# Kernel optimization log

Measured on AMD Instinct MI355X. Metric: run time of the kernel, lower is better.

Reference implementation:

```python
import jax, jax.numpy as jnp
import numpy as np

B, T, C, H = 4, 2048, 1024, 16
D = C // H


def setup_inputs() -> dict:
    key = jax.random.key(0)
    ks = jax.random.split(key, 5)
    s = C ** -0.5  # keep linear outputs O(1) like standard init
    x = jax.random.normal(ks[0], (B, T, C), dtype=jnp.float32)
    Wq = jax.random.normal(ks[1], (C, C), dtype=jnp.float32) * s
    Wk = jax.random.normal(ks[2], (C, C), dtype=jnp.float32) * s
    Wv = jax.random.normal(ks[3], (C, C), dtype=jnp.float32) * s
    Wproj = jax.random.normal(ks[4], (C, C), dtype=jnp.float32) * s
    alpha_raw = jnp.zeros((1, H, 1, 1), dtype=jnp.float32)
    beta_raw = jnp.zeros((1, H, 1, 1), dtype=jnp.float32)
    state = jnp.zeros((B, H, D, D), dtype=jnp.float32)
    return dict(x=x, Wq=Wq, Wk=Wk, Wv=Wv, Wproj=Wproj,
                alpha_raw=alpha_raw, beta_raw=beta_raw, state=state)


def reference(x, Wq, Wk, Wv, Wproj, alpha_raw, beta_raw, state):
    Bx, Tx, Cx = x.shape
    Hn = alpha_raw.shape[1]
    Dh = Cx // Hn
    # projections (torch Linear: x @ W^T), split heads -> (B, H, T, D)
    def proj(W):
        return (x @ W.T).reshape(Bx, Tx, Hn, Dh).transpose(0, 2, 1, 3)
    q, k, v = proj(Wq), proj(Wk), proj(Wv)
    # F.normalize(k, dim=-1) with eps=1e-12
    k = k / jnp.maximum(jnp.linalg.norm(k, axis=-1, keepdims=True), 1e-12)
    alpha = jax.nn.sigmoid(alpha_raw) * 0.5  # (1, H, 1, 1)
    beta = jax.nn.sigmoid(beta_raw) * 0.5

    def step(st, qkv):
        qt, kt, vt = qkv  # each (B, H, D)
        # y_t = q_t @ state^T
        y = jnp.einsum('bhe,bhde->bhd', qt, st)
        # Mk = state @ k_t
        Mk = jnp.einsum('bhde,bhe->bhd', st, kt)
        st = st - alpha * jnp.einsum('bhd,bhe->bhde', Mk, kt) \
                + beta * jnp.einsum('bhd,bhe->bhde', vt, kt)
        return st, y

    # scan over time: (T, B, H, D)
    qT = q.transpose(2, 0, 1, 3)
    kT = k.transpose(2, 0, 1, 3)
    vT = v.transpose(2, 0, 1, 3)
    state_f, ys = jax.lax.scan(step, state, (qT, kT, vT))
    y = ys.transpose(1, 0, 2, 3).reshape(Bx, Tx, Cx)  # (B, T, C)
    out = y @ Wproj.T
    return out, state_f
```

## Files before the change

kernel.cpp:

```cpp
#include <hip/hip_runtime.h>
#include <hip/hip_bf16.h>
#include <cstdint>

#define B_ 4
#define T_ 2048
#define C_ 1024
#define H_ 16
#define D_ 64
#define NC_ 32
#define L_ 64

typedef __attribute__((ext_vector_type(8))) short bf16x8;
typedef __attribute__((ext_vector_type(4))) float f32x4;

static __device__ __forceinline__ unsigned short f2bf(float f) {
  unsigned u = __float_as_uint(f);
  u += 0x7fff + ((u >> 16) & 1);
  return (unsigned short)(u >> 16);
}
static __device__ __forceinline__ float bf2f(unsigned short b) {
  return __uint_as_float(((unsigned)b) << 16);
}
static __device__ __forceinline__ int swz128(int row, int byte) {
  return row * 128 + (byte ^ ((row & 7) << 4));
}

#define LDS_BARRIER() asm volatile("s_waitcnt lgkmcnt(0)\ns_barrier" ::: "memory")

__global__ __launch_bounds__(256) void cvt_all(const float* __restrict__ x,
                                               const float* __restrict__ wq,
                                               const float* __restrict__ wk,
                                               const float* __restrict__ wv,
                                               const float* __restrict__ wp,
                                               unsigned short* __restrict__ xbf,
                                               unsigned short* __restrict__ W3,
                                               unsigned short* __restrict__ Wp) {
  const int bidx = blockIdx.x;
  const float* src;
  unsigned short* dst;
  long base;
  if (bidx < 8192) {
    src = x; dst = xbf; base = (long)bidx * 1024;
  } else {
    const int g = (bidx - 8192) >> 10;
    src = (g == 0) ? wq : (g == 1) ? wk : (g == 2) ? wv : wp;
    dst = (g < 3) ? (W3 + (long)g * 1048576) : Wp;
    base = (long)((bidx - 8192) & 1023) * 1024;
  }
  long i = base + threadIdx.x * 4;
  float4 v = *reinterpret_cast<const float4*>(src + i);
  ushort4 o;
  o.x = f2bf(v.x); o.y = f2bf(v.y); o.z = f2bf(v.z); o.w = f2bf(v.w);
  *reinterpret_cast<ushort4*>(dst + i) = o;
}

#define STAGE256(GP, GR0, KT, LOFF) do {                                          \
    const unsigned short* _s = (GP) + ((GR0) + wid * 8 + lr8) * 1024L             \
                               + (long)(KT) * 64 + skb * 8;                       \
    char* _d = (char*)lds + (LOFF) + wid * 1024;                                  \
    __builtin_amdgcn_global_load_lds((const __attribute__((address_space(1))) void*)_s,      \
        (__attribute__((address_space(3))) void*)_d, 16, 0, 0);                   \
    __builtin_amdgcn_global_load_lds((const __attribute__((address_space(1))) void*)(_s + 64 * 1024L), \
        (__attribute__((address_space(3))) void*)(_d + 8192), 16, 0, 0);          \
  } while (0)

#define PHASE256(AO, BO, MH, NH, STG) do {                                        \
    asm volatile("s_waitcnt vmcnt(6)" ::: "memory");                              \
    bf16x8 av[4][2], bv[2][2];                                                    \
    {                                                                             \
      const char* ab = (const char*)lds + (AO) + (MH) * 16384 + arow;             \
      const char* bb = (const char*)lds + (BO) + (NH) * 16384 + brow;             \
      _Pragma("unroll")                                                           \
      for (int j = 0; j < 4; ++j) {                                               \
        av[j][0] = *(const bf16x8*)(ab + j * 4096 + cb0);                         \
        av[j][1] = *(const bf16x8*)(ab + j * 4096 + cb1);                         \
      }                                                                           \
      _Pragma("unroll")                                                           \
      for (int j2 = 0; j2 < 2; ++j2) {                                            \
        bv[j2][0] = *(const bf16x8*)(bb + j2 * 8192 + cb0);                       \
        bv[j2][1] = *(const bf16x8*)(bb + j2 * 8192 + cb1);                       \
      }                                                                           \
    }                                                                             \
    STG;                                                                          \
    __builtin_amdgcn_s_barrier();                                                 \
    asm volatile("s_waitcnt lgkmcnt(0)" ::: "memory");                            \
    __builtin_amdgcn_sched_barrier(0);                                            \
    __builtin_amdgcn_s_setprio(1);                                                \
    _Pragma("unroll")                                                             \
    for (int j = 0; j < 4; ++j)                                                   \
      _Pragma("unroll")                                                           \
      for (int j2 = 0; j2 < 2; ++j2)                                              \
        acc[(MH) * 4 + j][(NH) * 2 + j2] = __builtin_amdgcn_mfma_f32_16x16x32_bf16( \
            av[j][0], bv[j2][0], acc[(MH) * 4 + j][(NH) * 2 + j2], 0, 0, 0);      \
    _Pragma("unroll")                                                             \
    for (int j = 0; j < 4; ++j)                                                   \
      _Pragma("unroll")                                                           \
      for (int j2 = 0; j2 < 2; ++j2)                                              \
        acc[(MH) * 4 + j][(NH) * 2 + j2] = __builtin_amdgcn_mfma_f32_16x16x32_bf16( \
            av[j][1], bv[j2][1], acc[(MH) * 4 + j][(NH) * 2 + j2], 0, 0, 0);      \
    __builtin_amdgcn_s_setprio(0);                                                \
    __builtin_amdgcn_s_barrier();                                                 \
  } while (0)

__global__ __launch_bounds__(512, 2) void gemm256_bt(
    const unsigned short* __restrict__ A,
    const unsigned short* __restrict__ Bw,
    unsigned short* __restrict__ C, int N) {
  __shared__ __align__(16) char lds[131072];
  enum { EA = 0, EB = 32768, OA = 65536, OB = 98304, HF = 16384 };
  const int tid = threadIdx.x;
  const int wid = tid >> 6, lane = tid & 63;
  const int wm = wid >> 2, wn = wid & 3;
  const int f = lane & 15, g = lane >> 4;
  const int lr8 = lane >> 3, lc = lane & 7;
  const int skb = lc ^ lr8;
  const int bid = blockIdx.y * gridDim.x + blockIdx.x;
  const int cpx = (gridDim.x * gridDim.y) >> 3;
  const int sw = (bid & 7) * cpx + (bid >> 3);
  const long bM = (long)(sw / gridDim.x) * 256;
  const long bN = (long)(sw % gridDim.x) * 256;
  const int cb0 = ((0 + g) ^ (f & 7)) * 16;
  const int cb1 = ((4 + g) ^ (f & 7)) * 16;
  const int arow = (wm * 16 + f) * 128;
  const int brow = (wn * 16 + f) * 128;

  f32x4 acc[8][4] = {};

  STAGE256(A, bM, 0, EA);
  STAGE256(Bw, bN, 0, EB);
  STAGE256(A, bM + 128, 0, EA + HF);
  STAGE256(Bw, bN + 128, 0, EB + HF);
  STAGE256(Bw, bN, 1, OB);
  STAGE256(A, bM, 1, OA);
  asm volatile("s_waitcnt vmcnt(8)" ::: "memory");
  __builtin_amdgcn_s_barrier();

  for (int i = 0; i < 8; ++i) {
    const int todd = 2 * i + 1;
    int te = 2 * i + 2; if (te > 14) te = 14;
    int to = 2 * i + 3; if (to > 15) to = 15;
    PHASE256(EA, EB, 0, 0, STAGE256(A, bM + 128, todd, OA + HF));
    PHASE256(EA, EB, 1, 0, STAGE256(Bw, bN + 128, todd, OB + HF));
    PHASE256(EA, EB, 0, 1, STAGE256(Bw, bN, te, EB));
    PHASE256(EA, EB, 1, 1, STAGE256(A, bM, te, EA));
    PHASE256(OA, OB, 0, 0, STAGE256(A, bM + 128, te, EA + HF));
    PHASE256(OA, OB, 1, 0, STAGE256(Bw, bN + 128, te, EB + HF));
    PHASE256(OA, OB, 0, 1, STAGE256(Bw, bN, to, OB));
    PHASE256(OA, OB, 1, 1, STAGE256(A, bM, to, OA));
  }

#pragma unroll
  for (int mf = 0; mf < 8; ++mf) {
    long row = bM + (mf >> 2) * 128 + (mf & 3) * 32 + wm * 16 + g * 4;
#pragma unroll
    for (int nf = 0; nf < 4; ++nf) {
      long col = bN + (nf >> 1) * 128 + (nf & 1) * 64 + wn * 16 + f;
#pragma unroll
      for (int r = 0; r < 4; ++r)
        C[(row + r) * (long)N + col] = f2bf(acc[mf][nf][r]);
    }
  }
}

template<int OUT_BF16>
__global__ __launch_bounds__(256) void gemm_bt(const unsigned short* __restrict__ A,
                                               const unsigned short* __restrict__ Bw,
                                               void* __restrict__ Cp,
                                               int M, int N, int K) {
  __shared__ __align__(16) unsigned short sA[128 * 32];
  __shared__ __align__(16) unsigned short sB[128 * 32];
  const int tid = threadIdx.x;
  const int wid = tid >> 6, lane = tid & 63;
  const int wm = wid >> 1, wn = wid & 1;
  const int bid = blockIdx.y * gridDim.x + blockIdx.x;
  const int cpx = (gridDim.x * gridDim.y) >> 3;
  const int sw = (bid & 7) * cpx + (bid >> 3);
  const long blockM = (long)(sw / gridDim.x) * 128;
  const long blockN = (long)(sw % gridDim.x) * 128;

  f32x4 acc[4][4] = {};

  const int ar = lane >> 2;
  const int ac = (lane & 3) * 8;
  const unsigned short* Abase = A + (blockM + wid * 32 + ar) * (long)K + ac;
  const unsigned short* Bbase = Bw + (blockN + wid * 32 + ar) * (long)K + ac;
  char* sAb = (char*)sA + wid * 2048;
  char* sBb = (char*)sB + wid * 2048;

  for (int k0 = 0; k0 < K; k0 += 32) {
    __syncthreads();
    __builtin_amdgcn_global_load_lds((const __attribute__((address_space(1))) void*)(Abase + k0),
                                     (__attribute__((address_space(3))) void*)(sAb), 16, 0, 0);
    __builtin_amdgcn_global_load_lds((const __attribute__((address_space(1))) void*)(Abase + 16 * (long)K + k0),
                                     (__attribute__((address_space(3))) void*)(sAb + 1024), 16, 0, 0);
    __builtin_amdgcn_global_load_lds((const __attribute__((address_space(1))) void*)(Bbase + k0),
                                     (__attribute__((address_space(3))) void*)(sBb), 16, 0, 0);
    __builtin_amdgcn_global_load_lds((const __attribute__((address_space(1))) void*)(Bbase + 16 * (long)K + k0),
                                     (__attribute__((address_space(3))) void*)(sBb + 1024), 16, 0, 0);
    __syncthreads();

    const int koff = (lane >> 4) * 8;
    const int rA = wm * 64 + (lane & 15);
    const int rB = wn * 64 + (lane & 15);
    bf16x8 af[4], bfr[4];
#pragma unroll
    for (int m = 0; m < 4; ++m)
      af[m] = *reinterpret_cast<const bf16x8*>(&sA[(rA + m * 16) * 32 + koff]);
#pragma unroll
    for (int n = 0; n < 4; ++n)
      bfr[n] = *reinterpret_cast<const bf16x8*>(&sB[(rB + n * 16) * 32 + koff]);
#pragma unroll
    for (int m = 0; m < 4; ++m)
#pragma unroll
      for (int n = 0; n < 4; ++n)
        acc[m][n] = __builtin_amdgcn_mfma_f32_16x16x32_bf16(af[m], bfr[n], acc[m][n], 0, 0, 0);
  }

  const int cr = (lane >> 4) * 4;
  const int cc = lane & 15;
#pragma unroll
  for (int m = 0; m < 4; ++m) {
    long R = blockM + wm * 64 + m * 16 + cr;
#pragma unroll
    for (int n = 0; n < 4; ++n) {
      long Cc = blockN + wn * 64 + n * 16 + cc;
#pragma unroll
      for (int r = 0; r < 4; ++r) {
        if (OUT_BF16)
          ((unsigned short*)Cp)[(R + r) * (long)N + Cc] = f2bf(acc[m][n][r]);
        else
          ((float*)Cp)[(R + r) * (long)N + Cc] = acc[m][n][r];
      }
    }
  }
}

__global__ __launch_bounds__(256) void chunk_prep(
    unsigned short* __restrict__ qkv,
    const float* __restrict__ a_raw, const float* __restrict__ b_raw,
    unsigned short* __restrict__ Ubuf, unsigned short* __restrict__ Wbuf,
    unsigned short* __restrict__ SLbuf) {
  __shared__ __align__(16) unsigned short sK[64 * 64];
  __shared__ __align__(16) unsigned short sQ[64 * 64];
  __shared__ __align__(16) unsigned short sV[64 * 64];
  __shared__ float sA[64 * 64];

  const int blk = blockIdx.x;
  const int bh = blk >> 5, c = blk & 31;
  const int b = bh >> 4, h = bh & 15;
  const int tid = threadIdx.x;
  const int wid = tid >> 6, lane = tid & 63;

  const float alpha = 0.5f / (1.f + __expf(-a_raw[h]));
  const float beta  = 0.5f / (1.f + __expf(-b_raw[h]));

  {
    const int row = tid >> 2, cg = tid & 3;
    unsigned short* gp = qkv + (long)(b * 2048 + c * 64 + row) * 3072 + h * 64 + cg * 16;
    bf16x8 q0 = *(const bf16x8*)(gp);
    bf16x8 q1 = *(const bf16x8*)(gp + 8);
    bf16x8 k0 = *(const bf16x8*)(gp + 1024);
    bf16x8 k1 = *(const bf16x8*)(gp + 1024 + 8);
    bf16x8 v0 = *(const bf16x8*)(gp + 2048);
    bf16x8 v1 = *(const bf16x8*)(gp + 2048 + 8);
    float kf[16];
    float ss = 0.f;
#pragma unroll
    for (int i = 0; i < 8; ++i) { kf[i] = bf2f((unsigned short)k0[i]); ss += kf[i] * kf[i]; }
#pragma unroll
    for (int i = 0; i < 8; ++i) { kf[8 + i] = bf2f((unsigned short)k1[i]); ss += kf[8 + i] * kf[8 + i]; }
    ss += __shfl_xor(ss, 1);
    ss += __shfl_xor(ss, 2);
    const float inv = 1.f / fmaxf(sqrtf(ss), 1e-12f);
    bf16x8 n0, n1;
#pragma unroll
    for (int i = 0; i < 8; ++i) { n0[i] = (short)f2bf(kf[i] * inv); n1[i] = (short)f2bf(kf[8 + i] * inv); }
    *(bf16x8*)((char*)sK + swz128(row, cg * 32)) = n0;
    *(bf16x8*)((char*)sK + swz128(row, cg * 32 + 16)) = n1;
    *(bf16x8*)((char*)sQ + swz128(row, cg * 32)) = q0;
    *(bf16x8*)((char*)sQ + swz128(row, cg * 32 + 16)) = q1;
    *(bf16x8*)((char*)sV + row * 128 + cg * 32) = v0;
    *(bf16x8*)((char*)sV + row * 128 + cg * 32 + 16) = v1;
  }
  __syncthreads();

  {
    const int erow = tid >> 2, tq = tid & 3;
    unsigned short kt[16];
#pragma unroll
    for (int i = 0; i < 16; ++i)
      kt[i] = *(const unsigned short*)((const char*)sK + swz128(tq * 16 + i, 2 * erow));
    unsigned short* vp = qkv + (long)(b * 2048 + c * 64 + erow) * 3072 + 2048 + h * 64 + tq * 16;
    *(bf16x8*)vp = *(const bf16x8*)kt;
    *(bf16x8*)(vp + 8) = *(const bf16x8*)(kt + 8);
  }

  const int rfrag = lane & 15, koff = (lane >> 4) * 8, crow = (lane >> 4) * 4;
  const int w2 = wid & 1;
  if (wid < 2) {
#pragma unroll
    for (int mt = 0; mt < 2; ++mt) {
      const int m = w2 * 2 + mt;
      const int ra = 16 * m + rfrag;
      f32x4 acc[4] = {};
#pragma unroll
      for (int ks = 0; ks < 2; ++ks) {
        bf16x8 af = *(const bf16x8*)((const char*)sK + swz128(ra, ks * 64 + koff * 2));
#pragma unroll
        for (int n = 0; n < 4; ++n) {
          bf16x8 bf = *(const bf16x8*)((const char*)sK + swz128(16 * n + rfrag, ks * 64 + koff * 2));
          acc[n] = __builtin_amdgcn_mfma_f32_16x16x32_bf16(af, bf, acc[n], 0, 0, 0);
        }
      }
#pragma unroll
      for (int n = 0; n < 4; ++n)
#pragma unroll
        for (int r = 0; r < 4; ++r)
          sA[(16 * m + crow + r) * 64 + 16 * n + rfrag] = acc[n][r];
    }
  } else {
#pragma unroll
    for (int mt = 0; mt < 2; ++mt) {
      const int m = w2 * 2 + mt;
      const int ra = 16 * m + rfrag;
      f32x4 acc[4] = {};
#pragma unroll
      for (int ks = 0; ks < 2; ++ks) {
        bf16x8 af = *(const bf16x8*)((const char*)sQ + swz128(ra, ks * 64 + koff * 2));
#pragma unroll
        for (int n = 0; n < 4; ++n) {
          bf16x8 bf = *(const bf16x8*)((const char*)sK + swz128(16 * n + rfrag, ks * 64 + koff * 2));
          acc[n] = __builtin_amdgcn_mfma_f32_16x16x32_bf16(af, bf, acc[n], 0, 0, 0);
        }
      }
#pragma unroll
      for (int n = 0; n < 4; ++n)
#pragma unroll
        for (int r = 0; r < 4; ++r) {
          int t = 16 * m + crow + r, j = 16 * n + rfrag;
          SLbuf[(long)blk * 4096 + t * 64 + j] = (j < t) ? f2bf(acc[n][r]) : (unsigned short)0;
        }
    }
  }
  __syncthreads();

  if (wid < 2) {
    const int d = lane;
    float x[64];
#pragma unroll
    for (int t = 0; t < 64; ++t) {
      float rhs;
      if (wid == 0) rhs = beta * bf2f(sV[t * 64 + d]);
      else          rhs = alpha * bf2f(*(const unsigned short*)((const char*)sK + swz128(t, 2 * d)));
      float s = 0.f;
#pragma unroll
      for (int j = 0; j < t; ++j) s = fmaf(sA[t * 64 + j], x[j], s);
      x[t] = rhs - alpha * s;
    }
    unsigned short* ob = (wid == 0 ? Ubuf : Wbuf) + (long)blk * 4096 + d;
#pragma unroll
    for (int t = 0; t < 64; ++t) ob[t * 64] = f2bf(x[t]);
  }
}

__global__ __launch_bounds__(256) void chunk_scan(
    const unsigned short* __restrict__ qkv,
    const unsigned short* __restrict__ Ubuf, const unsigned short* __restrict__ Wbuf,
    const unsigned short* __restrict__ SLbuf,
    const float* __restrict__ state_in, unsigned short* __restrict__ ybuf,
    float* __restrict__ state_out) {
  __shared__ __align__(16) char lds[73728];

  const int bid0 = blockIdx.x;
  const int blk = (bid0 & 7) * 32 + (bid0 >> 3);
  const int bh = blk >> 2, dq = blk & 3;
  const int b = bh >> 4, h = bh & 15;
  const int tid = threadIdx.x, wid = tid >> 6, lane = tid & 63;
  const int rfrag = lane & 15, koff = (lane >> 4) * 8, crow = (lane >> 4) * 4;
  const int row = tid >> 2, cg = tid & 3;

  char* gt = lds + 69632;
  char* ssb = lds + 71680;

  const unsigned short* gpb = qkv + (long)(b * 2048 + row) * 3072 + h * 64 + cg * 16;
  const long tbb = ((long)(bh * 32) * 64 + row) * 64 + cg * 16;
  const long ubb = ((long)(bh * 32) * 64 + (tid >> 1)) * 64 + dq * 16 + (tid & 1) * 8;

  bf16x8 qv0, qv1, kt0, kt1, wv0, wv1, sl0, sl1, uv;
#define LOADREGS(CN) do {                                                       \
    const unsigned short* gp = gpb + (long)(CN) * 64 * 3072;                    \
    const long tb = tbb + (long)(CN) * 4096;                                    \
    qv0 = *(const bf16x8*)gp;            qv1 = *(const bf16x8*)(gp + 8);        \
    kt0 = *(const bf16x8*)(gp + 2048);   kt1 = *(const bf16x8*)(gp + 2048 + 8); \
    wv0 = *(const bf16x8*)(Wbuf + tb);   wv1 = *(const bf16x8*)(Wbuf + tb + 8); \
    sl0 = *(const bf16x8*)(SLbuf + tb);  sl1 = *(const bf16x8*)(SLbuf + tb + 8);\
    if (tid < 128) uv = *(const bf16x8*)(Ubuf + ubb + (long)(CN) * 4096);       \
  } while (0)

#define WRITE_TILES(BUF) do {                                                   \
    char* bp = lds + (BUF) * 34816;                                             \
    *(bf16x8*)(bp + swz128(row, cg * 32)) = qv0;                                \
    *(bf16x8*)(bp + swz128(row, cg * 32 + 16)) = qv1;                           \
    *(bf16x8*)(bp + 8192 + swz128(row, cg * 32)) = wv0;                         \
    *(bf16x8*)(bp + 8192 + swz128(row, cg * 32 + 16)) = wv1;                    \
    *(bf16x8*)(bp + 16384 + swz128(row, cg * 32)) = sl0;                        \
    *(bf16x8*)(bp + 16384 + swz128(row, cg * 32 + 16)) = sl1;                   \
    *(bf16x8*)(bp + 24576 + swz128(row, cg * 32)) = kt0;                        \
    *(bf16x8*)(bp + 24576 + swz128(row, cg * 32 + 16)) = kt1;                   \
    if (tid < 128) *(bf16x8*)(bp + 32768 + ((tid >> 1) * 16 + (tid & 1) * 8) * 2) = uv; \
  } while (0)

  f32x4 sacc;
#pragma unroll
  for (int r = 0; r < 4; ++r)
    sacc[r] = state_in[(long)bh * 4096 + (dq * 16 + crow + r) * 64 + 16 * wid + rfrag];
#pragma unroll
  for (int r = 0; r < 4; ++r)
    *(unsigned short*)(ssb + swz128(crow + r, 2 * (16 * wid + rfrag))) = f2bf(sacc[r]);

  LOADREGS(0);
  WRITE_TILES(0);
  LOADREGS(1);
  LDS_BARRIER();

  for (int c = 0; c < NC_; ++c) {
    const int cur = c & 1;
    const char* bp = lds + cur * 34816;
    const int ta = 16 * wid + rfrag;

    f32x4 p = {};
    f32x4 yac = {};
#pragma unroll
    for (int ks = 0; ks < 2; ++ks) {
      bf16x8 afw = *(const bf16x8*)(bp + 8192 + swz128(ta, ks * 64 + koff * 2));
      bf16x8 afq = *(const bf16x8*)(bp + swz128(ta, ks * 64 + koff * 2));
      bf16x8 bS = *(const bf16x8*)(ssb + swz128(rfrag, ks * 64 + koff * 2));
      p = __builtin_amdgcn_mfma_f32_16x16x32_bf16(afw, bS, p, 0, 0, 0);
      yac = __builtin_amdgcn_mfma_f32_16x16x32_bf16(afq, bS, yac, 0, 0, 0);
    }
#pragma unroll
    for (int r = 0; r < 4; ++r) {
      int t = 16 * wid + crow + r;
      float gg = bf2f(*(const unsigned short*)(bp + 32768 + (t * 16 + rfrag) * 2)) - p[r];
      *(unsigned short*)(gt + swz128(rfrag, 2 * t)) = f2bf(gg);
    }
    LDS_BARRIER();

#pragma unroll
    for (int ks = 0; ks < 2; ++ks) {
      bf16x8 aSL = *(const bf16x8*)(bp + 16384 + swz128(ta, ks * 64 + koff * 2));
      bf16x8 bGT = *(const bf16x8*)(gt + swz128(rfrag, ks * 64 + koff * 2));
      yac = __builtin_amdgcn_mfma_f32_16x16x32_bf16(aSL, bGT, yac, 0, 0, 0);
    }
#pragma unroll
    for (int ks = 0; ks < 2; ++ks) {
      bf16x8 aGT = *(const bf16x8*)(gt + swz128(rfrag, ks * 64 + koff * 2));
      bf16x8 bKT = *(const bf16x8*)(bp + 24576 + swz128(16 * wid + rfrag, ks * 64 + koff * 2));
      sacc = __builtin_amdgcn_mfma_f32_16x16x32_bf16(aGT, bKT, sacc, 0, 0, 0);
    }
#pragma unroll
    for (int r = 0; r < 4; ++r) {
      int t = 16 * wid + crow + r;
      ybuf[(long)(b * 2048 + c * 64 + t) * 1024 + h * 64 + dq * 16 + rfrag] = f2bf(yac[r]);
    }
#pragma unroll
    for (int r = 0; r < 4; ++r)
      *(unsigned short*)(ssb + swz128(crow + r, 2 * (16 * wid + rfrag))) = f2bf(sacc[r]);
    if (c + 1 < NC_) {
      WRITE_TILES(cur ^ 1);
      int cn = c + 2; if (cn > NC_ - 1) cn = NC_ - 1;
      LOADREGS(cn);
    }
    LDS_BARRIER();
  }

#pragma unroll
  for (int r = 0; r < 4; ++r)
    state_out[(long)bh * 4096 + (dq * 16 + crow + r) * 64 + 16 * wid + rfrag] = sacc[r];
#undef LOADREGS
#undef WRITE_TILES
}

extern "C" void kernel_launch(void* const* d_in, const int* in_sizes, int n_in,
                              void* d_out, int out_size, void* d_ws, size_t ws_size,
                              hipStream_t stream) {
  (void)in_sizes; (void)n_in; (void)out_size; (void)ws_size;
  const float* x     = (const float*)d_in[0];
  const float* Wq    = (const float*)d_in[1];
  const float* Wk    = (const float*)d_in[2];
  const float* Wv    = (const float*)d_in[3];
  const float* Wproj = (const float*)d_in[4];
  const float* a_raw = (const float*)d_in[5];
  const float* b_raw = (const float*)d_in[6];
  const float* state = (const float*)d_in[7];

  char* ws = (char*)d_ws;
  unsigned short* xbf = (unsigned short*)ws;
  unsigned short* W3  = (unsigned short*)(ws + (16l << 20));
  unsigned short* Wp  = (unsigned short*)(ws + (22l << 20));
  unsigned short* qkv = (unsigned short*)(ws + (24l << 20));
  unsigned short* Ub  = (unsigned short*)(ws + (72l << 20));
  unsigned short* Wb  = (unsigned short*)(ws + (88l << 20));
  unsigned short* SLb = (unsigned short*)(ws + (104l << 20));
  float* out = (float*)d_out;
  float* state_out = out + (long)B_ * T_ * C_;

  cvt_all<<<dim3(12288), dim3(256), 0, stream>>>(x, Wq, Wk, Wv, Wproj, xbf, W3, Wp);

  gemm256_bt<<<dim3(3072 / 256, 8192 / 256), dim3(512), 0, stream>>>(xbf, W3, qkv, 3072);

  chunk_prep<<<dim3(2048), dim3(256), 0, stream>>>(qkv, a_raw, b_raw, Ub, Wb, SLb);
  chunk_scan<<<dim3(256), dim3(256), 0, stream>>>(qkv, Ub, Wb, SLb, state, xbf, state_out);

  gemm_bt<0><<<dim3(1024 / 128, 8192 / 128), dim3(256), 0, stream>>>(xbf, Wp, (void*)out, 8192, 1024, 1024);
}
```

Baseline: 180.8 us.

## Merge four d-quarter scan blocks per head into one 1024-thread block sharing tiles

The chunk scan previously launched 256 blocks of 256 threads, with four blocks per (batch, head) each redundantly loading the same Q, K, W and SL chunk tiles. It now launches 64 blocks of 1024 threads, one per (batch, head). The four d-quarters run as wave groups within the block and share one copy of the staged tiles, and each thread loads a single tile slice. This removes the fourfold redundant global loads and LDS staging. In exchange only 64 CUs are used, the block-wide barriers now span 16 waves, and LDS use per block grows.

```diff
diff --git a/kernel.cpp b/kernel.cpp
--- a/kernel.cpp
+++ b/kernel.cpp
@@ -363,60 +363,59 @@
   }
 }
 
-__global__ __launch_bounds__(256) void chunk_scan(
+__global__ __launch_bounds__(1024) void chunk_scan(
     const unsigned short* __restrict__ qkv,
     const unsigned short* __restrict__ Ubuf, const unsigned short* __restrict__ Wbuf,
     const unsigned short* __restrict__ SLbuf,
     const float* __restrict__ state_in, unsigned short* __restrict__ ybuf,
     float* __restrict__ state_out) {
-  __shared__ __align__(16) char lds[73728];
+  __shared__ __align__(16) char lds[98304];
 
   const int bid0 = blockIdx.x;
-  const int blk = (bid0 & 7) * 32 + (bid0 >> 3);
-  const int bh = blk >> 2, dq = blk & 3;
+  const int bh = (bid0 & 7) * 8 + (bid0 >> 3);
   const int b = bh >> 4, h = bh & 15;
-  const int tid = threadIdx.x, wid = tid >> 6, lane = tid & 63;
+  const int tid = threadIdx.x;
+  const int wid = tid >> 6, lane = tid & 63;
+  const int dq = wid >> 2, w4 = wid & 3;
   const int rfrag = lane & 15, koff = (lane >> 4) * 8, crow = (lane >> 4) * 4;
-  const int row = tid >> 2, cg = tid & 3;
-
-  char* gt = lds + 69632;
-  char* ssb = lds + 71680;
-
-  const unsigned short* gpb = qkv + (long)(b * 2048 + row) * 3072 + h * 64 + cg * 16;
-  const long tbb = ((long)(bh * 32) * 64 + row) * 64 + cg * 16;
-  const long ubb = ((long)(bh * 32) * 64 + (tid >> 1)) * 64 + dq * 16 + (tid & 1) * 8;
-
-  bf16x8 qv0, qv1, kt0, kt1, wv0, wv1, sl0, sl1, uv;
+
+  const int stile = tid >> 8, srow = (tid >> 2) & 63, scg = tid & 3;
+  const int tg = tid & 255, ur = tg >> 1, uh = tg & 1;
+
+  char* gt  = lds + 81920 + dq * 2048;
+  char* ssb = lds + 90112 + dq * 2048;
+
+  const unsigned short* gsrc0;
+  long gstride;
+  if (stile == 0)      { gsrc0 = qkv + (long)(b * 2048 + srow) * 3072 + h * 64 + scg * 16; gstride = 64 * 3072; }
+  else if (stile == 1) { gsrc0 = Wbuf + ((long)(bh * 32) * 64 + srow) * 64 + scg * 16; gstride = 4096; }
+  else if (stile == 2) { gsrc0 = SLbuf + ((long)(bh * 32) * 64 + srow) * 64 + scg * 16; gstride = 4096; }
+  else                 { gsrc0 = qkv + (long)(b * 2048 + srow) * 3072 + 2048 + h * 64 + scg * 16; gstride = 64 * 3072; }
+  const unsigned short* usrc0 = Ubuf + ((long)(bh * 32) * 64 + ur) * 64 + dq * 16 + uh * 8;
+
+  bf16x8 rv0 = {}, rv1 = {}, uv = {};
 #define LOADREGS(CN) do {                                                       \
-    const unsigned short* gp = gpb + (long)(CN) * 64 * 3072;                    \
-    const long tb = tbb + (long)(CN) * 4096;                                    \
-    qv0 = *(const bf16x8*)gp;            qv1 = *(const bf16x8*)(gp + 8);        \
-    kt0 = *(const bf16x8*)(gp + 2048);   kt1 = *(const bf16x8*)(gp + 2048 + 8); \
-    wv0 = *(const bf16x8*)(Wbuf + tb);   wv1 = *(const bf16x8*)(Wbuf + tb + 8); \
-    sl0 = *(const bf16x8*)(SLbuf + tb);  sl1 = *(const bf16x8*)(SLbuf + tb + 8);\
-    if (tid < 128) uv = *(const bf16x8*)(Ubuf + ubb + (long)(CN) * 4096);       \
+    const unsigned short* gp = gsrc0 + (long)(CN) * gstride;                    \
+    rv0 = *(const bf16x8*)gp;                                                   \
+    rv1 = *(const bf16x8*)(gp + 8);                                             \
+    if (tg < 128) uv = *(const bf16x8*)(usrc0 + (long)(CN) * 4096);             \
   } while (0)
 
 #define WRITE_TILES(BUF) do {                                                   \
-    char* bp = lds + (BUF) * 34816;                                             \
-    *(bf16x8*)(bp + swz128(row, cg * 32)) = qv0;                                \
-    *(bf16x8*)(bp + swz128(row, cg * 32 + 16)) = qv1;                           \
-    *(bf16x8*)(bp + 8192 + swz128(row, cg * 32)) = wv0;                         \
-    *(bf16x8*)(bp + 8192 + swz128(row, cg * 32 + 16)) = wv1;                    \
-    *(bf16x8*)(bp + 16384 + swz128(row, cg * 32)) = sl0;                        \
-    *(bf16x8*)(bp + 16384 + swz128(row, cg * 32 + 16)) = sl1;                   \
-    *(bf16x8*)(bp + 24576 + swz128(row, cg * 32)) = kt0;                        \
-    *(bf16x8*)(bp + 24576 + swz128(row, cg * 32 + 16)) = kt1;                   \
-    if (tid < 128) *(bf16x8*)(bp + 32768 + ((tid >> 1) * 16 + (tid & 1) * 8) * 2) = uv; \
+    char* bp_ = lds + (BUF) * 32768 + stile * 8192;                             \
+    *(bf16x8*)(bp_ + swz128(srow, scg * 32)) = rv0;                             \
+    *(bf16x8*)(bp_ + swz128(srow, scg * 32 + 16)) = rv1;                        \
+    if (tg < 128)                                                               \
+      *(bf16x8*)(lds + 65536 + dq * 4096 + (BUF) * 2048 + (ur * 16 + uh * 8) * 2) = uv; \
   } while (0)
 
   f32x4 sacc;
 #pragma unroll
   for (int r = 0; r < 4; ++r)
-    sacc[r] = state_in[(long)bh * 4096 + (dq * 16 + crow + r) * 64 + 16 * wid + rfrag];
+    sacc[r] = state_in[(long)bh * 4096 + (dq * 16 + crow + r) * 64 + 16 * w4 + rfrag];
 #pragma unroll
   for (int r = 0; r < 4; ++r)
-    *(unsigned short*)(ssb + swz128(crow + r, 2 * (16 * wid + rfrag))) = f2bf(sacc[r]);
+    *(unsigned short*)(ssb + swz128(crow + r, 2 * (16 * w4 + rfrag))) = f2bf(sacc[r]);
 
   LOADREGS(0);
   WRITE_TILES(0);
@@ -425,8 +424,9 @@
 
   for (int c = 0; c < NC_; ++c) {
     const int cur = c & 1;
-    const char* bp = lds + cur * 34816;
-    const int ta = 16 * wid + rfrag;
+    const char* bp = lds + cur * 32768;
+    const char* up = lds + 65536 + dq * 4096 + cur * 2048;
+    const int ta = 16 * w4 + rfrag;
 
     f32x4 p = {};
     f32x4 yac = {};
@@ -440,8 +440,8 @@
     }
 #pragma unroll
     for (int r = 0; r < 4; ++r) {
-      int t = 16 * wid + crow + r;
-      float gg = bf2f(*(const unsigned short*)(bp + 32768 + (t * 16 + rfrag) * 2)) - p[r];
+      int t = 16 * w4 + crow + r;
+      float gg = bf2f(*(const unsigned short*)(up + (t * 16 + rfrag) * 2)) - p[r];
       *(unsigned short*)(gt + swz128(rfrag, 2 * t)) = f2bf(gg);
     }
     LDS_BARRIER();
@@ -455,17 +455,17 @@
 #pragma unroll
     for (int ks = 0; ks < 2; ++ks) {
       bf16x8 aGT = *(const bf16x8*)(gt + swz128(rfrag, ks * 64 + koff * 2));
-      bf16x8 bKT = *(const bf16x8*)(bp + 24576 + swz128(16 * wid + rfrag, ks * 64 + koff * 2));
+      bf16x8 bKT = *(const bf16x8*)(bp + 24576 + swz128(16 * w4 + rfrag, ks * 64 + koff * 2));
       sacc = __builtin_amdgcn_mfma_f32_16x16x32_bf16(aGT, bKT, sacc, 0, 0, 0);
     }
 #pragma unroll
     for (int r = 0; r < 4; ++r) {
-      int t = 16 * wid + crow + r;
+      int t = 16 * w4 + crow + r;
       ybuf[(long)(b * 2048 + c * 64 + t) * 1024 + h * 64 + dq * 16 + rfrag] = f2bf(yac[r]);
     }
 #pragma unroll
     for (int r = 0; r < 4; ++r)
-      *(unsigned short*)(ssb + swz128(crow + r, 2 * (16 * wid + rfrag))) = f2bf(sacc[r]);
+      *(unsigned short*)(ssb + swz128(crow + r, 2 * (16 * w4 + rfrag))) = f2bf(sacc[r]);
     if (c + 1 < NC_) {
       WRITE_TILES(cur ^ 1);
       int cn = c + 2; if (cn > NC_ - 1) cn = NC_ - 1;
@@ -476,7 +476,7 @@
 
 #pragma unroll
   for (int r = 0; r < 4; ++r)
-    state_out[(long)bh * 4096 + (dq * 16 + crow + r) * 64 + 16 * wid + rfrag] = sacc[r];
+    state_out[(long)bh * 4096 + (dq * 16 + crow + r) * 64 + 16 * w4 + rfrag] = sacc[r];
 #undef LOADREGS
 #undef WRITE_TILES
 }
@@ -510,7 +510,7 @@
   gemm256_bt<<<dim3(3072 / 256, 8192 / 256), dim3(512), 0, stream>>>(xbf, W3, qkv, 3072);
 
   chunk_prep<<<dim3(2048), dim3(256), 0, stream>>>(qkv, a_raw, b_raw, Ub, Wb, SLb);
-  chunk_scan<<<dim3(256), dim3(256), 0, stream>>>(qkv, Ub, Wb, SLb, state, xbf, state_out);
+  chunk_scan<<<dim3(64), dim3(1024), 0, stream>>>(qkv, Ub, Wb, SLb, state, xbf, state_out);
 
   gemm_bt<0><<<dim3(1024 / 128, 8192 / 128), dim3(256), 0, stream>>>(xbf, Wp, (void*)out, 8192, 1024, 1024);
 }
```

Measured after the change: 194.3 us. 7.5% more time.

## Unify both GEMMs on a 128x256 double-buffered MFMA kernel template

Applied to the files above, without the earlier changes.

Replaces the 256x256 QKV GEMM and the simple 128x128 output-projection GEMM with one templated 128x256 tile kernel. It uses 512 threads, a two-stage LDS double buffer with global_load_lds, and vmcnt(0) waits every two phases. The QKV GEMM gets twice as many blocks and fewer accumulator registers per thread, trading operand reuse per tile for more parallelism. The output projection moves from a single-buffered 128x128 kernel with a barrier every 32-wide K step to the pipelined kernel, though that launch now has only 256 blocks.

```diff
diff --git a/kernel.cpp b/kernel.cpp
--- a/kernel.cpp
+++ b/kernel.cpp
@@ -26,6 +26,7 @@
 }
 
 #define LDS_BARRIER() asm volatile("s_waitcnt lgkmcnt(0)\ns_barrier" ::: "memory")
+#define VMCNT0 asm volatile("s_waitcnt vmcnt(0)" ::: "memory");
 
 __global__ __launch_bounds__(256) void cvt_all(const float* __restrict__ x,
                                                const float* __restrict__ wq,
@@ -54,7 +55,8 @@
   *reinterpret_cast<ushort4*>(dst + i) = o;
 }
 
-#define STAGE256(GP, GR0, KT, LOFF) do {                                          \
+
+#define STAGEH(GP, GR0, KT, LOFF) do {                                            \
     const unsigned short* _s = (GP) + ((GR0) + wid * 8 + lr8) * 1024L             \
                                + (long)(KT) * 64 + skb * 8;                       \
     char* _d = (char*)lds + (LOFF) + wid * 1024;                                  \
@@ -64,11 +66,10 @@
         (__attribute__((address_space(3))) void*)(_d + 8192), 16, 0, 0);          \
   } while (0)
 
-#define PHASE256(AO, BO, MH, NH, STG) do {                                        \
-    asm volatile("s_waitcnt vmcnt(6)" ::: "memory");                              \
+#define PHASE4(AO, BO, NH, STG, ENDVM) do {                                       \
     bf16x8 av[4][2], bv[2][2];                                                    \
     {                                                                             \
-      const char* ab = (const char*)lds + (AO) + (MH) * 16384 + arow;             \
+      const char* ab = (const char*)lds + (AO) + arow;                            \
       const char* bb = (const char*)lds + (BO) + (NH) * 16384 + brow;             \
       _Pragma("unroll")                                                           \
       for (int j = 0; j < 4; ++j) {                                               \
@@ -90,24 +91,26 @@
     for (int j = 0; j < 4; ++j)                                                   \
       _Pragma("unroll")                                                           \
       for (int j2 = 0; j2 < 2; ++j2)                                              \
-        acc[(MH) * 4 + j][(NH) * 2 + j2] = __builtin_amdgcn_mfma_f32_16x16x32_bf16( \
-            av[j][0], bv[j2][0], acc[(MH) * 4 + j][(NH) * 2 + j2], 0, 0, 0);      \
+        acc[j][(NH) * 2 + j2] = __builtin_amdgcn_mfma_f32_16x16x32_bf16(          \
+            av[j][0], bv[j2][0], acc[j][(NH) * 2 + j2], 0, 0, 0);                 \
     _Pragma("unroll")                                                             \
     for (int j = 0; j < 4; ++j)                                                   \
       _Pragma("unroll")                                                           \
       for (int j2 = 0; j2 < 2; ++j2)                                              \
-        acc[(MH) * 4 + j][(NH) * 2 + j2] = __builtin_amdgcn_mfma_f32_16x16x32_bf16( \
-            av[j][1], bv[j2][1], acc[(MH) * 4 + j][(NH) * 2 + j2], 0, 0, 0);      \
+        acc[j][(NH) * 2 + j2] = __builtin_amdgcn_mfma_f32_16x16x32_bf16(          \
+            av[j][1], bv[j2][1], acc[j][(NH) * 2 + j2], 0, 0, 0);                 \
     __builtin_amdgcn_s_setprio(0);                                                \
+    ENDVM                                                                         \
     __builtin_amdgcn_s_barrier();                                                 \
   } while (0)
 
-__global__ __launch_bounds__(512, 2) void gemm256_bt(
+template<int OUT_BF16>
+__global__ __launch_bounds__(512, 2) void gemm128x256(
     const unsigned short* __restrict__ A,
     const unsigned short* __restrict__ Bw,
-    unsigned short* __restrict__ C, int N) {
-  __shared__ __align__(16) char lds[131072];
-  enum { EA = 0, EB = 32768, OA = 65536, OB = 98304, HF = 16384 };
+    void* __restrict__ Cp, int N) {
+  __shared__ __align__(16) char lds[98304];
+  enum { EA = 0, EB = 16384, OA = 49152, OB = 65536 };
   const int tid = threadIdx.x;
   const int wid = tid >> 6, lane = tid & 63;
   const int wm = wid >> 2, wn = wid & 3;
@@ -117,119 +120,46 @@
   const int bid = blockIdx.y * gridDim.x + blockIdx.x;
   const int cpx = (gridDim.x * gridDim.y) >> 3;
   const int sw = (bid & 7) * cpx + (bid >> 3);
-  const long bM = (long)(sw / gridDim.x) * 256;
+  const long bM = (long)(sw / gridDim.x) * 128;
   const long bN = (long)(sw % gridDim.x) * 256;
   const int cb0 = ((0 + g) ^ (f & 7)) * 16;
   const int cb1 = ((4 + g) ^ (f & 7)) * 16;
   const int arow = (wm * 16 + f) * 128;
   const int brow = (wn * 16 + f) * 128;
 
-  f32x4 acc[8][4] = {};
-
-  STAGE256(A, bM, 0, EA);
-  STAGE256(Bw, bN, 0, EB);
-  STAGE256(A, bM + 128, 0, EA + HF);
-  STAGE256(Bw, bN + 128, 0, EB + HF);
-  STAGE256(Bw, bN, 1, OB);
-  STAGE256(A, bM, 1, OA);
-  asm volatile("s_waitcnt vmcnt(8)" ::: "memory");
+  f32x4 acc[4][4] = {};
+
+  STAGEH(Bw, bN, 0, EB);
+  STAGEH(Bw, bN + 128, 0, EB + 16384);
+  STAGEH(A, bM, 0, EA);
+  VMCNT0
   __builtin_amdgcn_s_barrier();
 
   for (int i = 0; i < 8; ++i) {
-    const int todd = 2 * i + 1;
-    int te = 2 * i + 2; if (te > 14) te = 14;
-    int to = 2 * i + 3; if (to > 15) to = 15;
-    PHASE256(EA, EB, 0, 0, STAGE256(A, bM + 128, todd, OA + HF));
-    PHASE256(EA, EB, 1, 0, STAGE256(Bw, bN + 128, todd, OB + HF));
-    PHASE256(EA, EB, 0, 1, STAGE256(Bw, bN, te, EB));
-    PHASE256(EA, EB, 1, 1, STAGE256(A, bM, te, EA));
-    PHASE256(OA, OB, 0, 0, STAGE256(A, bM + 128, te, EA + HF));
-    PHASE256(OA, OB, 1, 0, STAGE256(Bw, bN + 128, te, EB + HF));
-    PHASE256(OA, OB, 0, 1, STAGE256(Bw, bN, to, OB));
-    PHASE256(OA, OB, 1, 1, STAGE256(A, bM, to, OA));
-  }
-
-#pragma unroll
-  for (int mf = 0; mf < 8; ++mf) {
-    long row = bM + (mf >> 2) * 128 + (mf & 3) * 32 + wm * 16 + g * 4;
+    const int to = 2 * i + 1;
+    const int te = 2 * i + 2;
+    PHASE4(EA, EB, 0,
+           { STAGEH(Bw, bN, to, OB); STAGEH(Bw, bN + 128, to, OB + 16384); STAGEH(A, bM, to, OA); },
+           );
+    PHASE4(EA, EB, 1, {}, VMCNT0);
+    PHASE4(OA, OB, 0,
+           { if (i < 7) { STAGEH(Bw, bN, te, EB); STAGEH(Bw, bN + 128, te, EB + 16384); STAGEH(A, bM, te, EA); } },
+           );
+    PHASE4(OA, OB, 1, {}, VMCNT0);
+  }
+
+#pragma unroll
+  for (int mf = 0; mf < 4; ++mf) {
+    long row = bM + mf * 32 + wm * 16 + g * 4;
 #pragma unroll
     for (int nf = 0; nf < 4; ++nf) {
       long col = bN + (nf >> 1) * 128 + (nf & 1) * 64 + wn * 16 + f;
 #pragma unroll
-      for (int r = 0; r < 4; ++r)
-        C[(row + r) * (long)N + col] = f2bf(acc[mf][nf][r]);
-    }
-  }
-}
-
-template<int OUT_BF16>
-__global__ __launch_bounds__(256) void gemm_bt(const unsigned short* __restrict__ A,
-                                               const unsigned short* __restrict__ Bw,
-                                               void* __restrict__ Cp,
-                                               int M, int N, int K) {
-  __shared__ __align__(16) unsigned short sA[128 * 32];
-  __shared__ __align__(16) unsigned short sB[128 * 32];
-  const int tid = threadIdx.x;
-  const int wid = tid >> 6, lane = tid & 63;
-  const int wm = wid >> 1, wn = wid & 1;
-  const int bid = blockIdx.y * gridDim.x + blockIdx.x;
-  const int cpx = (gridDim.x * gridDim.y) >> 3;
-  const int sw = (bid & 7) * cpx + (bid >> 3);
-  const long blockM = (long)(sw / gridDim.x) * 128;
-  const long blockN = (long)(sw % gridDim.x) * 128;
-
-  f32x4 acc[4][4] = {};
-
-  const int ar = lane >> 2;
-  const int ac = (lane & 3) * 8;
-  const unsigned short* Abase = A + (blockM + wid * 32 + ar) * (long)K + ac;
-  const unsigned short* Bbase = Bw + (blockN + wid * 32 + ar) * (long)K + ac;
-  char* sAb = (char*)sA + wid * 2048;
-  char* sBb = (char*)sB + wid * 2048;
-
-  for (int k0 = 0; k0 < K; k0 += 32) {
-    __syncthreads();
-    __builtin_amdgcn_global_load_lds((const __attribute__((address_space(1))) void*)(Abase + k0),
-                                     (__attribute__((address_space(3))) void*)(sAb), 16, 0, 0);
-    __builtin_amdgcn_global_load_lds((const __attribute__((address_space(1))) void*)(Abase + 16 * (long)K + k0),
-                                     (__attribute__((address_space(3))) void*)(sAb + 1024), 16, 0, 0);
-    __builtin_amdgcn_global_load_lds((const __attribute__((address_space(1))) void*)(Bbase + k0),
-                                     (__attribute__((address_space(3))) void*)(sBb), 16, 0, 0);
-    __builtin_amdgcn_global_load_lds((const __attribute__((address_space(1))) void*)(Bbase + 16 * (long)K + k0),
-                                     (__attribute__((address_space(3))) void*)(sBb + 1024), 16, 0, 0);
-    __syncthreads();
-
-    const int koff = (lane >> 4) * 8;
-    const int rA = wm * 64 + (lane & 15);
-    const int rB = wn * 64 + (lane & 15);
-    bf16x8 af[4], bfr[4];
-#pragma unroll
-    for (int m = 0; m < 4; ++m)
-      af[m] = *reinterpret_cast<const bf16x8*>(&sA[(rA + m * 16) * 32 + koff]);
-#pragma unroll
-    for (int n = 0; n < 4; ++n)
-      bfr[n] = *reinterpret_cast<const bf16x8*>(&sB[(rB + n * 16) * 32 + koff]);
-#pragma unroll
-    for (int m = 0; m < 4; ++m)
-#pragma unroll
-      for (int n = 0; n < 4; ++n)
-        acc[m][n] = __builtin_amdgcn_mfma_f32_16x16x32_bf16(af[m], bfr[n], acc[m][n], 0, 0, 0);
-  }
-
-  const int cr = (lane >> 4) * 4;
-  const int cc = lane & 15;
-#pragma unroll
-  for (int m = 0; m < 4; ++m) {
-    long R = blockM + wm * 64 + m * 16 + cr;
-#pragma unroll
-    for (int n = 0; n < 4; ++n) {
-      long Cc = blockN + wn * 64 + n * 16 + cc;
-#pragma unroll
       for (int r = 0; r < 4; ++r) {
         if (OUT_BF16)
-          ((unsigned short*)Cp)[(R + r) * (long)N + Cc] = f2bf(acc[m][n][r]);
+          ((unsigned short*)Cp)[(row + r) * (long)N + col] = f2bf(acc[mf][nf][r]);
         else
-          ((float*)Cp)[(R + r) * (long)N + Cc] = acc[m][n][r];
+          ((float*)Cp)[(row + r) * (long)N + col] = acc[mf][nf][r];
       }
     }
   }
@@ -398,16 +328,16 @@
   } while (0)
 
 #define WRITE_TILES(BUF) do {                                                   \
-    char* bp = lds + (BUF) * 34816;                                             \
-    *(bf16x8*)(bp + swz128(row, cg * 32)) = qv0;                                \
-    *(bf16x8*)(bp + swz128(row, cg * 32 + 16)) = qv1;                           \
-    *(bf16x8*)(bp + 8192 + swz128(row, cg * 32)) = wv0;                         \
-    *(bf16x8*)(bp + 8192 + swz128(row, cg * 32 + 16)) = wv1;                    \
-    *(bf16x8*)(bp + 16384 + swz128(row, cg * 32)) = sl0;                        \
-    *(bf16x8*)(bp + 16384 + swz128(row, cg * 32 + 16)) = sl1;                   \
-    *(bf16x8*)(bp + 24576 + swz128(row, cg * 32)) = kt0;                        \
-    *(bf16x8*)(bp + 24576 + swz128(row, cg * 32 + 16)) = kt1;                   \
-    if (tid < 128) *(bf16x8*)(bp + 32768 + ((tid >> 1) * 16 + (tid & 1) * 8) * 2) = uv; \
+    char* bp_ = lds + (BUF) * 34816;                                            \
+    *(bf16x8*)(bp_ + swz128(row, cg * 32)) = qv0;                               \
+    *(bf16x8*)(bp_ + swz128(row, cg * 32 + 16)) = qv1;                          \
+    *(bf16x8*)(bp_ + 8192 + swz128(row, cg * 32)) = wv0;                        \
+    *(bf16x8*)(bp_ + 8192 + swz128(row, cg * 32 + 16)) = wv1;                   \
+    *(bf16x8*)(bp_ + 16384 + swz128(row, cg * 32)) = sl0;                       \
+    *(bf16x8*)(bp_ + 16384 + swz128(row, cg * 32 + 16)) = sl1;                  \
+    *(bf16x8*)(bp_ + 24576 + swz128(row, cg * 32)) = kt0;                       \
+    *(bf16x8*)(bp_ + 24576 + swz128(row, cg * 32 + 16)) = kt1;                  \
+    if (tid < 128) *(bf16x8*)(bp_ + 32768 + ((tid >> 1) * 16 + (tid & 1) * 8) * 2) = uv; \
   } while (0)
 
   f32x4 sacc;
@@ -507,10 +437,10 @@
 
   cvt_all<<<dim3(12288), dim3(256), 0, stream>>>(x, Wq, Wk, Wv, Wproj, xbf, W3, Wp);
 
-  gemm256_bt<<<dim3(3072 / 256, 8192 / 256), dim3(512), 0, stream>>>(xbf, W3, qkv, 3072);
+  gemm128x256<1><<<dim3(3072 / 256, 8192 / 128), dim3(512), 0, stream>>>(xbf, W3, (void*)qkv, 3072);
 
   chunk_prep<<<dim3(2048), dim3(256), 0, stream>>>(qkv, a_raw, b_raw, Ub, Wb, SLb);
   chunk_scan<<<dim3(256), dim3(256), 0, stream>>>(qkv, Ub, Wb, SLb, state, xbf, state_out);
 
-  gemm_bt<0><<<dim3(1024 / 128, 8192 / 128), dim3(256), 0, stream>>>(xbf, Wp, (void*)out, 8192, 1024, 1024);
-}
+  gemm128x256<0><<<dim3(1024 / 256, 8192 / 128), dim3(512), 0, stream>>>(xbf, Wp, (void*)out, 1024);
+}
```

After: 176.6 us. 1.02x faster.
